# Optimization experiments

Hardware: AMD Instinct MI355X
Metric: run time of the kernel (lower is better)

The kernel has to match this reference:

```python
import jax, jax.numpy as jnp
import numpy as np


def setup_inputs() -> dict:
    key = jax.random.key(0)
    k1, k2, k3, k4, k5 = jax.random.split(key, 5)
    B, S, H = 64, 2048, 512
    enc = jax.random.normal(k1, (B, S, H), dtype=jnp.float32)
    fin = jax.random.normal(k2, (B, H), dtype=jnp.float32)
    # nn.Linear(2H, H): weight [H, 2H]; nn.Linear(H, 1, bias=False): weight [1, H]
    attn_w = jax.random.normal(k3, (H, 2 * H), dtype=jnp.float32) * (1.0 / np.sqrt(2 * H))
    attn_b = jax.random.normal(k4, (H,), dtype=jnp.float32) * 0.01
    v_w = jax.random.normal(k5, (1, H), dtype=jnp.float32) * (1.0 / np.sqrt(H))
    return {"encoder_outputs": enc, "final_hidden": fin,
            "attn_w": attn_w, "attn_b": attn_b, "v_w": v_w}


def reference(encoder_outputs, final_hidden, attn_w, attn_b, v_w):
    # Split attn_w into the encoder part and final-hidden part to avoid
    # materializing the [B, S, 2H] concat tensor (same math as concat+linear).
    H = final_hidden.shape[-1]
    w_enc = attn_w[:, :H]   # [H, H]
    w_fin = attn_w[:, H:]   # [H, H]
    # energy: [B, S, H]
    e_enc = jnp.einsum('bsh,kh->bsk', encoder_outputs, w_enc)
    e_fin = jnp.einsum('bh,kh->bk', final_hidden, w_fin)
    energy = jnp.tanh(e_enc + e_fin[:, None, :] + attn_b)
    scores = jnp.einsum('bsk,k->bs', energy, v_w[0])      # [B, S]
    weights = jax.nn.softmax(scores, axis=1)              # [B, S]
    context = jnp.einsum('bs,bsh->bh', weights, encoder_outputs)  # [B, H]
    return context
```

## Files before the change

### kernel.cpp

```cpp
#include <hip/hip_runtime.h>
#include <hip/hip_bf16.h>

#define BATCH 64
#define SEQ   2048
#define HID   512
#define ROWS  (BATCH * SEQ)

typedef __attribute__((ext_vector_type(8))) short short8;
typedef __attribute__((ext_vector_type(4))) float f32x4;

#define GLOBAL_AS __attribute__((address_space(1)))
#define LDS_AS    __attribute__((address_space(3)))

__device__ __forceinline__ void g2l16(const void* g, void* l) {
    __builtin_amdgcn_global_load_lds((const GLOBAL_AS unsigned int*)g,
                                     (LDS_AS unsigned int*)l, 16, 0, 0);
}

__device__ inline unsigned int cvt2_bf16(float x, float y) {
    __hip_bfloat162 h = __float22bfloat162_rn(make_float2(x, y));
    union { __hip_bfloat162 h2; unsigned int u; } u;
    u.h2 = h;
    return u.u;
}

__device__ inline float fast_tanh(float x) {
    float e = __expf(2.0f * x);
    return 1.0f - 2.0f / (e + 1.0f);
}

__global__ void k_prep2(const float* __restrict__ attw, const float* __restrict__ attb,
                        const float* __restrict__ fin, unsigned short* __restrict__ wb,
                        float* __restrict__ cbuf) {
    int bid = blockIdx.x;
    int t   = threadIdx.x;
    if (bid < 128) {
        size_t e = ((size_t)bid * 256 + t) * 8;
        int k = (int)(e >> 9);
        int h = (int)(e & 511);
        const float* g = attw + (size_t)k * (2 * HID) + h;
        float4 a0 = *(const float4*)g;
        float4 a1 = *(const float4*)(g + 4);
        uint4 p = {cvt2_bf16(a0.x, a0.y), cvt2_bf16(a0.z, a0.w),
                   cvt2_bf16(a1.x, a1.y), cvt2_bf16(a1.z, a1.w)};
        *(uint4*)(wb + (size_t)k * HID + h) = p;
    } else {
        int fb = bid - 128;
        int b  = fb >> 4;
        int k  = (fb & 15) * 32 + (t >> 3);
        int l8 = t & 7;
        const float* f = fin + b * HID;
        const float* w = attw + (size_t)k * (2 * HID) + HID;
        float s = 0.0f;
        for (int h = l8 * 4; h < HID; h += 32) {
            float4 a  = *(const float4*)(f + h);
            float4 ww = *(const float4*)(w + h);
            s += a.x * ww.x + a.y * ww.y + a.z * ww.z + a.w * ww.w;
        }
        s += __shfl_xor(s, 1);
        s += __shfl_xor(s, 2);
        s += __shfl_xor(s, 4);
        if (l8 == 0) cbuf[b * HID + k] = s + attb[k];
    }
}

__global__ __launch_bounds__(256, 2) void k_energy_f(
        const float* __restrict__ enc, const unsigned short* __restrict__ wb,
        const float* __restrict__ cbuf, const float* __restrict__ vw,
        float* __restrict__ num, float* __restrict__ ml) {
    __shared__ __align__(16) unsigned short As[64 * 64];
    __shared__ __align__(16) unsigned short Bs[512 * 64];

    const int sRow = blockIdx.x * 64;
    const int bIdx = sRow >> 11;
    const int t    = threadIdx.x;
    const int lane = t & 63;
    const int wave = t >> 6;
    const int l16  = lane & 15;
    const int q    = lane >> 4;

    const int tr = t >> 2;
    const int tc = (t & 3) * 16;
    const int c0 = (t & 3) * 2;

    const int lr  = lane >> 3;
    const int lc  = lane & 7;
    const int swz = lc ^ lr;

    const float* gA = enc + (size_t)(sRow + tr) * HID + tc;
    const unsigned short* gB = wb + (size_t)(wave * 128 + lr) * HID + swz * 8;

    f32x4 acc[4][8];
    #pragma unroll
    for (int i = 0; i < 4; ++i)
        #pragma unroll
        for (int j = 0; j < 8; ++j) acc[i][j] = (f32x4){0.f, 0.f, 0.f, 0.f};

    for (int h0 = 0; h0 < HID; h0 += 64) {
        float4 a0 = *(const float4*)(gA + h0);
        float4 a1 = *(const float4*)(gA + h0 + 4);
        float4 a2 = *(const float4*)(gA + h0 + 8);
        float4 a3 = *(const float4*)(gA + h0 + 12);
        #pragma unroll
        for (int j = 0; j < 16; ++j)
            g2l16(gB + (size_t)(j * 8) * HID + h0, Bs + (wave * 128 + j * 8) * 64);
        uint4 p0 = {cvt2_bf16(a0.x, a0.y), cvt2_bf16(a0.z, a0.w),
                    cvt2_bf16(a1.x, a1.y), cvt2_bf16(a1.z, a1.w)};
        uint4 p1 = {cvt2_bf16(a2.x, a2.y), cvt2_bf16(a2.z, a2.w),
                    cvt2_bf16(a3.x, a3.y), cvt2_bf16(a3.z, a3.w)};
        *(uint4*)(&As[tr * 64 + ((c0    ) ^ (tr & 7)) * 8]) = p0;
        *(uint4*)(&As[tr * 64 + ((c0 + 1) ^ (tr & 7)) * 8]) = p1;
        __syncthreads();

        #pragma unroll
        for (int kk = 0; kk < 64; kk += 32) {
            short8 af[4], bf[8];
            const int cb = (kk >> 3) + q;
            #pragma unroll
            for (int i = 0; i < 4; ++i) {
                int row = i * 16 + l16;
                af[i] = *(const short8*)(&As[row * 64 + (cb ^ (row & 7)) * 8]);
            }
            #pragma unroll
            for (int j = 0; j < 8; ++j) {
                int row = wave * 128 + j * 16 + l16;
                bf[j] = *(const short8*)(&Bs[row * 64 + (cb ^ (row & 7)) * 8]);
            }
            #pragma unroll
            for (int i = 0; i < 4; ++i)
                #pragma unroll
                for (int j = 0; j < 8; ++j)
                    acc[i][j] = __builtin_amdgcn_mfma_f32_16x16x32_bf16(
                        af[i], bf[j], acc[i][j], 0, 0, 0);
        }
        __syncthreads();
    }

    float* ssc = (float*)As;
    float* wsm = (float*)As + 64;

    if (t < 64) ssc[t] = 0.0f;
    __syncthreads();

    float cv[8], vv[8];
    #pragma unroll
    for (int j = 0; j < 8; ++j) {
        int c = wave * 128 + j * 16 + l16;
        cv[j] = cbuf[bIdx * HID + c];
        vv[j] = vw[c];
    }

    #pragma unroll
    for (int i = 0; i < 4; ++i) {
        #pragma unroll
        for (int r = 0; r < 4; ++r) {
            float sum = 0.0f;
            #pragma unroll
            for (int j = 0; j < 8; ++j)
                sum += fast_tanh(acc[i][j][r] + cv[j]) * vv[j];
            sum += __shfl_xor(sum, 1);
            sum += __shfl_xor(sum, 2);
            sum += __shfl_xor(sum, 4);
            sum += __shfl_xor(sum, 8);
            if (l16 == 0) atomicAdd(&ssc[i * 16 + q * 4 + r], sum);
        }
    }
    __syncthreads();

    if (t < 64) {
        float x  = ssc[t];
        float mx = x;
        #pragma unroll
        for (int m = 1; m < 64; m <<= 1) mx = fmaxf(mx, __shfl_xor(mx, m));
        float p = __expf(x - mx);
        float l = p;
        #pragma unroll
        for (int m = 1; m < 64; m <<= 1) l += __shfl_xor(l, m);
        wsm[t] = p;
        if (t == 0) ((float2*)ml)[blockIdx.x] = make_float2(mx, l);
    }
    __syncthreads();

    const float* e2 = enc + (size_t)sRow * HID + t * 2;
    float ax = 0.0f, ay = 0.0f;
    #pragma unroll 8
    for (int s = 0; s < 64; ++s) {
        float p  = wsm[s];
        float2 v = *(const float2*)(e2 + (size_t)s * HID);
        ax += p * v.x;
        ay += p * v.y;
    }
    *(float2*)(num + (size_t)blockIdx.x * HID + t * 2) = make_float2(ax, ay);
}

__global__ void k_combine(const float* __restrict__ num, const float* __restrict__ ml,
                          float* __restrict__ out) {
    int b = blockIdx.x;
    int t = threadIdx.x;
    __shared__ float sm[32], sl[32], sc[32];
    __shared__ float sM;
    if (t < 32) {
        float2 v = ((const float2*)ml)[b * 32 + t];
        sm[t] = v.x;
        sl[t] = v.y;
    }
    __syncthreads();
    if (t == 0) {
        float M = -1e30f;
        for (int i = 0; i < 32; ++i) M = fmaxf(M, sm[i]);
        sM = M;
    }
    __syncthreads();
    if (t < 32) sc[t] = __expf(sm[t] - sM);
    __syncthreads();
    float L = 0.0f;
    #pragma unroll
    for (int i = 0; i < 32; ++i) L += sc[i] * sl[i];
    float inv = 1.0f / L;
    const float* n = num + (size_t)b * 32 * HID + t;
    float a0 = 0.0f, a1 = 0.0f;
    #pragma unroll
    for (int i = 0; i < 32; ++i) {
        a0 += sc[i] * n[(size_t)i * HID];
        a1 += sc[i] * n[(size_t)i * HID + 256];
    }
    out[b * HID + t]       = a0 * inv;
    out[b * HID + t + 256] = a1 * inv;
}

#define BK  64
#define LDA 72

__global__ __launch_bounds__(256) void k_energy_fb(
        const float* __restrict__ enc, const float* __restrict__ attw,
        const float* __restrict__ cbuf, const float* __restrict__ vw,
        float* __restrict__ scores) {
    __shared__ __align__(16) unsigned short As[128 * LDA];
    __shared__ __align__(16) unsigned short Bs[128 * LDA];
    const int nTile = blockIdx.x * 128;
    const int sRow  = blockIdx.y * 128;
    const int bIdx  = sRow >> 11;
    const int t = threadIdx.x, lane = t & 63, wave = t >> 6;
    const int wm = wave >> 1, wn = wave & 1, l16 = lane & 15, q = lane >> 4;
    const int tr = t >> 3, tc = (t & 7) * 8;

    f32x4 acc[4][4];
    #pragma unroll
    for (int i = 0; i < 4; ++i)
        #pragma unroll
        for (int j = 0; j < 4; ++j) acc[i][j] = (f32x4){0.f, 0.f, 0.f, 0.f};

    for (int h0 = 0; h0 < HID; h0 += BK) {
        #pragma unroll
        for (int i = 0; i < 4; ++i) {
            int row = tr + i * 32;
            const float* gA = enc + (size_t)(sRow + row) * HID + h0 + tc;
            float4 a0 = *(const float4*)gA;
            float4 a1 = *(const float4*)(gA + 4);
            uint4 pa = {cvt2_bf16(a0.x, a0.y), cvt2_bf16(a0.z, a0.w),
                        cvt2_bf16(a1.x, a1.y), cvt2_bf16(a1.z, a1.w)};
            *(uint4*)(&As[row * LDA + tc]) = pa;
            const float* gB = attw + (size_t)(nTile + row) * (2 * HID) + h0 + tc;
            float4 b0 = *(const float4*)gB;
            float4 b1 = *(const float4*)(gB + 4);
            uint4 pb = {cvt2_bf16(b0.x, b0.y), cvt2_bf16(b0.z, b0.w),
                        cvt2_bf16(b1.x, b1.y), cvt2_bf16(b1.z, b1.w)};
            *(uint4*)(&Bs[row * LDA + tc]) = pb;
        }
        __syncthreads();
        #pragma unroll
        for (int kk = 0; kk < BK; kk += 32) {
            short8 af[4], bf[4];
            #pragma unroll
            for (int i = 0; i < 4; ++i)
                af[i] = *(const short8*)(&As[(wm * 64 + i * 16 + l16) * LDA + kk + q * 8]);
            #pragma unroll
            for (int j = 0; j < 4; ++j)
                bf[j] = *(const short8*)(&Bs[(wn * 64 + j * 16 + l16) * LDA + kk + q * 8]);
            #pragma unroll
            for (int i = 0; i < 4; ++i)
                #pragma unroll
                for (int j = 0; j < 4; ++j)
                    acc[i][j] = __builtin_amdgcn_mfma_f32_16x16x32_bf16(
                        af[i], bf[j], acc[i][j], 0, 0, 0);
        }
        __syncthreads();
    }
    #pragma unroll
    for (int i = 0; i < 4; ++i) {
        #pragma unroll
        for (int r = 0; r < 4; ++r) {
            float sum = 0.0f;
            #pragma unroll
            for (int j = 0; j < 4; ++j) {
                int colg = nTile + wn * 64 + j * 16 + l16;
                sum += fast_tanh(acc[i][j][r] + cbuf[bIdx * HID + colg]) * vw[colg];
            }
            sum += __shfl_xor(sum, 1);
            sum += __shfl_xor(sum, 2);
            sum += __shfl_xor(sum, 4);
            sum += __shfl_xor(sum, 8);
            if (l16 == 0) atomicAdd(&scores[sRow + wm * 64 + i * 16 + q * 4 + r], sum);
        }
    }
}

__global__ void k_softmax(float* __restrict__ sw) {
    int b = blockIdx.x;
    float* s = sw + (size_t)b * SEQ;
    int t = threadIdx.x;
    __shared__ float red[4];
    float lmax = -1e30f;
    for (int i = t; i < SEQ; i += 256) lmax = fmaxf(lmax, s[i]);
    for (int m = 1; m < 64; m <<= 1) lmax = fmaxf(lmax, __shfl_xor(lmax, m));
    if ((t & 63) == 0) red[t >> 6] = lmax;
    __syncthreads();
    float gmax = fmaxf(fmaxf(red[0], red[1]), fmaxf(red[2], red[3]));
    __syncthreads();
    float lsum = 0.0f;
    for (int i = t; i < SEQ; i += 256) lsum += __expf(s[i] - gmax);
    for (int m = 1; m < 64; m <<= 1) lsum += __shfl_xor(lsum, m);
    if ((t & 63) == 0) red[t >> 6] = lsum;
    __syncthreads();
    float inv = 1.0f / (red[0] + red[1] + red[2] + red[3]);
    for (int i = t; i < SEQ; i += 256) s[i] = __expf(s[i] - gmax) * inv;
}

__global__ void k_fin_fb(const float* __restrict__ fin, const float* __restrict__ attw,
                         const float* __restrict__ attb, float* __restrict__ cbuf) {
    int b  = blockIdx.y;
    int k  = blockIdx.x * 32 + (threadIdx.x >> 3);
    int l8 = threadIdx.x & 7;
    const float* f = fin + b * HID;
    const float* w = attw + (size_t)k * (2 * HID) + HID;
    float s = 0.0f;
    for (int h = l8 * 4; h < HID; h += 32) {
        float4 a  = *(const float4*)(f + h);
        float4 ww = *(const float4*)(w + h);
        s += a.x * ww.x + a.y * ww.y + a.z * ww.z + a.w * ww.w;
    }
    s += __shfl_xor(s, 1);
    s += __shfl_xor(s, 2);
    s += __shfl_xor(s, 4);
    if (l8 == 0) cbuf[b * HID + k] = s + attb[k];
}

__global__ void k_context_fb(const float* __restrict__ enc, const float* __restrict__ wts,
                             float* __restrict__ out) {
    int b = blockIdx.y, sc = blockIdx.x, t = threadIdx.x;
    const float* e = enc + ((size_t)b * SEQ + sc * 128) * HID + t * 2;
    const float* w = wts + (size_t)b * SEQ + sc * 128;
    float ax = 0.f, ay = 0.f;
    #pragma unroll 4
    for (int s = 0; s < 128; ++s) {
        float ws = w[s];
        float2 v = *(const float2*)(e + (size_t)s * HID);
        ax += ws * v.x;
        ay += ws * v.y;
    }
    atomicAdd(&out[b * HID + t * 2], ax);
    atomicAdd(&out[b * HID + t * 2 + 1], ay);
}

extern "C" void kernel_launch(void* const* d_in, const int* in_sizes, int n_in,
                              void* d_out, int out_size, void* d_ws, size_t ws_size,
                              hipStream_t stream) {
    const float* enc  = (const float*)d_in[0];
    const float* fin  = (const float*)d_in[1];
    const float* attw = (const float*)d_in[2];
    const float* attb = (const float*)d_in[3];
    const float* vw   = (const float*)d_in[4];
    float* out = (float*)d_out;

    char* ws = (char*)d_ws;
    float* cbuf        = (float*)ws;
    unsigned short* wb = (unsigned short*)(ws + 131072);
    float* num         = (float*)(ws + 131072 + 524288);
    float* mlb         = (float*)(ws + 131072 + 524288 + 4194304);
    const size_t need = 131072ull + 524288 + 4194304 + 16384;

    if (ws_size >= need) {
        k_prep2<<<1152, 256, 0, stream>>>(attw, attb, fin, wb, cbuf);
        k_energy_f<<<ROWS / 64, 256, 0, stream>>>(enc, wb, cbuf, vw, num, mlb);
        k_combine<<<BATCH, 256, 0, stream>>>(num, mlb, out);
    } else {
        float* sp = (float*)(ws + 131072);
        hipMemsetAsync(out, 0, (size_t)BATCH * HID * sizeof(float), stream);
        hipMemsetAsync(sp, 0, (size_t)ROWS * sizeof(float), stream);
        k_fin_fb<<<dim3(16, 64), 256, 0, stream>>>(fin, attw, attb, cbuf);
        k_energy_fb<<<dim3(4, ROWS / 128), 256, 0, stream>>>(enc, attw, cbuf, vw, sp);
        k_softmax<<<BATCH, 256, 0, stream>>>(sp);
        k_context_fb<<<dim3(16, 64), 256, 0, stream>>>(enc, sp, out);
    }
}
```

Before: 443.5 us.

## Halve B-tile LDS footprint by splitting output columns into two passes

The weight tile in shared memory drops from 512x64 to 256x64 bf16. Each K-step now loads and multiplies two 256-column halves in sequence, which lets the launch bounds go from 2 to 4 blocks per CU. The column-to-wave mapping changes so each wave covers 64 columns in each half, and the epilogue's cbuf and vw indexing is updated to match. In exchange it adds two extra barriers per K iteration, reloads A fragments from LDS twice, and the 128-float accumulator may not fit the tighter register budget, which could cause spills.

```diff
diff --git a/kernel.cpp b/kernel.cpp
--- a/kernel.cpp
+++ b/kernel.cpp
@@ -64,12 +64,12 @@
     }
 }
 
-__global__ __launch_bounds__(256, 2) void k_energy_f(
+__global__ __launch_bounds__(256, 4) void k_energy_f(
         const float* __restrict__ enc, const unsigned short* __restrict__ wb,
         const float* __restrict__ cbuf, const float* __restrict__ vw,
         float* __restrict__ num, float* __restrict__ ml) {
     __shared__ __align__(16) unsigned short As[64 * 64];
-    __shared__ __align__(16) unsigned short Bs[512 * 64];
+    __shared__ __align__(16) unsigned short Bs[256 * 64];
 
     const int sRow = blockIdx.x * 64;
     const int bIdx = sRow >> 11;
@@ -88,7 +88,7 @@
     const int swz = lc ^ lr;
 
     const float* gA = enc + (size_t)(sRow + tr) * HID + tc;
-    const unsigned short* gB = wb + (size_t)(wave * 128 + lr) * HID + swz * 8;
+    const unsigned short* gB = wb + (size_t)(wave * 64 + lr) * HID + swz * 8;
 
     f32x4 acc[4][8];
     #pragma unroll
@@ -102,8 +102,8 @@
         float4 a2 = *(const float4*)(gA + h0 + 8);
         float4 a3 = *(const float4*)(gA + h0 + 12);
         #pragma unroll
-        for (int j = 0; j < 16; ++j)
-            g2l16(gB + (size_t)(j * 8) * HID + h0, Bs + (wave * 128 + j * 8) * 64);
+        for (int j = 0; j < 8; ++j)
+            g2l16(gB + (size_t)(j * 8) * HID + h0, Bs + (wave * 64 + j * 8) * 64);
         uint4 p0 = {cvt2_bf16(a0.x, a0.y), cvt2_bf16(a0.z, a0.w),
                     cvt2_bf16(a1.x, a1.y), cvt2_bf16(a1.z, a1.w)};
         uint4 p1 = {cvt2_bf16(a2.x, a2.y), cvt2_bf16(a2.z, a2.w),
@@ -114,7 +114,7 @@
 
         #pragma unroll
         for (int kk = 0; kk < 64; kk += 32) {
-            short8 af[4], bf[8];
+            short8 af[4], bf[4];
             const int cb = (kk >> 3) + q;
             #pragma unroll
             for (int i = 0; i < 4; ++i) {
@@ -122,18 +122,46 @@
                 af[i] = *(const short8*)(&As[row * 64 + (cb ^ (row & 7)) * 8]);
             }
             #pragma unroll
-            for (int j = 0; j < 8; ++j) {
-                int row = wave * 128 + j * 16 + l16;
+            for (int j = 0; j < 4; ++j) {
+                int row = wave * 64 + j * 16 + l16;
                 bf[j] = *(const short8*)(&Bs[row * 64 + (cb ^ (row & 7)) * 8]);
             }
             #pragma unroll
             for (int i = 0; i < 4; ++i)
                 #pragma unroll
-                for (int j = 0; j < 8; ++j)
+                for (int j = 0; j < 4; ++j)
                     acc[i][j] = __builtin_amdgcn_mfma_f32_16x16x32_bf16(
                         af[i], bf[j], acc[i][j], 0, 0, 0);
         }
         __syncthreads();
+
+        #pragma unroll
+        for (int j = 0; j < 8; ++j)
+            g2l16(gB + (size_t)(256 + j * 8) * HID + h0, Bs + (wave * 64 + j * 8) * 64);
+        __syncthreads();
+
+        #pragma unroll
+        for (int kk = 0; kk < 64; kk += 32) {
+            short8 af[4], bf[4];
+            const int cb = (kk >> 3) + q;
+            #pragma unroll
+            for (int i = 0; i < 4; ++i) {
+                int row = i * 16 + l16;
+                af[i] = *(const short8*)(&As[row * 64 + (cb ^ (row & 7)) * 8]);
+            }
+            #pragma unroll
+            for (int j = 0; j < 4; ++j) {
+                int row = wave * 64 + j * 16 + l16;
+                bf[j] = *(const short8*)(&Bs[row * 64 + (cb ^ (row & 7)) * 8]);
+            }
+            #pragma unroll
+            for (int i = 0; i < 4; ++i)
+                #pragma unroll
+                for (int j = 0; j < 4; ++j)
+                    acc[i][4 + j] = __builtin_amdgcn_mfma_f32_16x16x32_bf16(
+                        af[i], bf[j], acc[i][4 + j], 0, 0, 0);
+        }
+        __syncthreads();
     }
 
     float* ssc = (float*)As;
@@ -144,11 +172,13 @@
 
     float cv[8], vv[8];
     #pragma unroll
-    for (int j = 0; j < 8; ++j) {
-        int c = wave * 128 + j * 16 + l16;
-        cv[j] = cbuf[bIdx * HID + c];
-        vv[j] = vw[c];
-    }
+    for (int h = 0; h < 2; ++h)
+        #pragma unroll
+        for (int j = 0; j < 4; ++j) {
+            int c = h * 256 + wave * 64 + j * 16 + l16;
+            cv[h * 4 + j] = cbuf[bIdx * HID + c];
+            vv[h * 4 + j] = vw[c];
+        }
 
     #pragma unroll
     for (int i = 0; i < 4; ++i) {
```

Result: slower. 876.9 us (+97.7%).
